# Performance work log

Hardware: AMD Instinct MI355X
Metric: run time of the kernel (lower is better)

Reference implementation:

```python
import jax, jax.numpy as jnp
import numpy as np

SAMPLE_NUMS = 9
VIEW_RANGE = 2      # args.max_turn_view_range
TEMP = 0.07         # args.temperature
AVG_EPS = 1e-6      # BertAVG eps
COS_EPS = 1e-8      # torch.cosine_similarity eps


def setup_inputs() -> dict:
    key = jax.random.key(0)
    k0, k1, k2 = jax.random.split(key, 3)
    G, S, H = 8, 512, 768            # groups, max_seq_length, hidden_size
    B = G * SAMPLE_NUMS              # 72 flattened dialogues
    self_output = jax.random.normal(k0, (B, S, H), dtype=jnp.float32)
    attention_mask = jnp.ones((B, S), dtype=jnp.float32)
    qa_ids = jax.random.randint(k1, (B, S), 0, 4, dtype=jnp.int32)
    turn_ids = jnp.sort(jax.random.randint(k2, (B, S), 0, 16, dtype=jnp.int32), axis=-1)
    labels = jnp.zeros((G, SAMPLE_NUMS), dtype=jnp.float32).at[:, 0].set(1.0)
    return {"self_output": self_output, "attention_mask": attention_mask,
            "labels": labels, "qa_ids": qa_ids, "turn_ids": turn_ids}


def _masked_avg(x, m):
    # BertAVG: sum over seq of x*m / (sum(m) + eps)   x:[B,S,H] m:[B,S]
    return jnp.sum(x * m[..., None], axis=1) / (jnp.sum(m, axis=1, keepdims=True) + AVG_EPS)


def _cos(x, y):
    # torch.cosine_similarity over last dim, eps-clamped norms
    dot = jnp.sum(x * y, axis=-1)
    nx = jnp.maximum(jnp.linalg.norm(x, axis=-1), COS_EPS)
    ny = jnp.maximum(jnp.linalg.norm(y, axis=-1), COS_EPS)
    c = dot / (nx * ny)
    c = jnp.where(c == 1.0, jnp.nan, c)   # cos[cos==1] = nan
    return c / TEMP


def _calc_loss(pred, labels):
    return -jnp.nanmean(jax.nn.log_softmax(pred, axis=-1) * labels)


def reference(self_output, attention_mask, labels, qa_ids, turn_ids):
    H = self_output.shape[-1]
    # role masks from qa_ids
    q_mask = ((qa_ids == 1) | (qa_ids == 2)).astype(self_output.dtype)
    a_mask = ((qa_ids == 0) | (qa_ids == 2)).astype(self_output.dtype)
    n_mask = (qa_ids == 3).astype(self_output.dtype)
    q_am = attention_mask * q_mask
    a_am = attention_mask * a_mask
    n_am = attention_mask * n_mask
    q_so = self_output * q_am[..., None]   # [B,S,H]
    a_so = self_output * a_am[..., None]
    n_so = self_output * n_am[..., None]
    # role-masked cross scores [B,S,S]
    q_w = jnp.einsum('bsh,bth->bst', q_so, a_so + n_so)
    a_w = jnp.einsum('bsh,bth->bst', a_so, q_so + n_so)
    n_w = jnp.einsum('bsh,bth->bst', n_so, q_so + a_so)
    # turn-range band mask: |turn_s - turn_t| <= range
    dt = turn_ids[:, :, None] - turn_ids[:, None, :]
    band = (jnp.abs(dt) <= VIEW_RANGE).astype(self_output.dtype)  # [B,S,S]
    filtered_w = (q_w + a_w + n_w) * band
    # cross outputs
    q_co = jnp.einsum('bst,bth->bsh', filtered_w, q_so)
    a_co = jnp.einsum('bst,bth->bsh', filtered_w, a_so)
    n_co = jnp.einsum('bst,bth->bsh', filtered_w, n_so)
    # masked averages
    q_self = _masked_avg(q_so, q_am)
    q_cross = _masked_avg(q_co, a_am + n_am)
    a_self = _masked_avg(a_so, a_am)
    a_cross = _masked_avg(a_co, q_am + n_am)
    n_self = _masked_avg(n_so, n_am)
    n_cross = _masked_avg(n_co, q_am + a_am)
    # [G, sample_nums, H]
    q_self = q_self.reshape(-1, SAMPLE_NUMS, H)
    q_cross = q_cross.reshape(-1, SAMPLE_NUMS, H)
    a_self = a_self.reshape(-1, SAMPLE_NUMS, H)
    a_cross = a_cross.reshape(-1, SAMPLE_NUMS, H)
    n_self = n_self.reshape(-1, SAMPLE_NUMS, H)
    n_cross = n_cross.reshape(-1, SAMPLE_NUMS, H)
    q_output = q_self[:, 0, :]
    a_output = a_self[:, 0, :]
    n_output = n_self[:, 0, :]
    # vectorized over sample axis (replaces the python loop + stack)
    logit_q = _cos(q_self, q_cross)  # [G, sample_nums]
    logit_a = _cos(a_self, a_cross)
    logit_n = _cos(n_self, n_cross)
    stage_loss = (_calc_loss(logit_a, labels) + _calc_loss(logit_q, labels)
                  + _calc_loss(logit_n, labels)) / 3.0
    return (stage_loss, q_output, a_output, n_output)
```

## Files before the change

### kernel.cpp

```cpp
#include <hip/hip_runtime.h>
#include <math.h>

#define BB 72
#define SS 512
#define HH 768
#define GG 8
#define SN 9
#define VR 2
#define NT 16
#define NPART 16


__device__ float g_G [(size_t)BB * NT * 4 * HH];
__device__ float g_Wm[(size_t)BB * NT * 4 * HH];
__device__ float g_snum[BB * 3 * HH];
__device__ float g_xpart[(size_t)BB * NPART * 3 * HH];
__device__ float g_logits[3 * BB];

__device__ __forceinline__ void class_masks(float am, int id, float& qv, float& av, float& nv) {
    qv = (id == 1 || id == 2) ? am : 0.0f;
    av = (id == 0 || id == 2) ? am : 0.0f;
    nv = (id == 3) ? am : 0.0f;
}

__global__ __launch_bounds__(384) void k_g(const float* __restrict__ x,
                                           const float* __restrict__ am,
                                           const int* __restrict__ qa,
                                           const int* __restrict__ turn) {
    __shared__ int   tn[SS];
    __shared__ float c2s[SS];
    __shared__ int   idvs[SS];
    __shared__ float Gh[4 * HH];

    const int u = blockIdx.x, b = blockIdx.y;
    const int tid = threadIdx.x;
    const int grp = (tid >= 192) ? 1 : 0;
    const int lt  = tid - grp * 192;

    for (int i = tid; i < SS; i += 384) tn[i] = turn[b * SS + i];
    __syncthreads();

    int L = 0, R = SS;
    while (L < R) { int m = (L + R) >> 1; if (tn[m] < u) L = m + 1; else R = m; }
    const int beg = L;
    L = beg; R = SS;
    while (L < R) { int m = (L + R) >> 1; if (tn[m] <= u) L = m + 1; else R = m; }
    const int end = L;

    for (int i = beg + tid; i < end; i += 384) {
        float a = am[b * SS + i]; c2s[i] = a * a;
        idvs[i] = qa[b * SS + i];
    }
    __syncthreads();

    float4 acc[4];
#pragma unroll
    for (int i = 0; i < 4; ++i) acc[i] = make_float4(0.f, 0.f, 0.f, 0.f);

    const float* xb = x + (size_t)b * SS * HH + lt * 4;
    for (int s0 = beg; s0 < end; s0 += 16) {
        float4 v[8];
#pragma unroll
        for (int k = 0; k < 8; ++k) {
            const int ss = s0 + 2 * k + grp;
            v[k] = (ss < end) ? *(const float4*)(xb + (size_t)ss * HH)
                              : make_float4(0.f, 0.f, 0.f, 0.f);
        }
#pragma unroll
        for (int k = 0; k < 8; ++k) {
            const int ss = s0 + 2 * k + grp;
            if (ss < end) {
                const float cc = c2s[ss];
                const int id = idvs[ss];
                const float4 xv = v[k];
                if (id == 0) { acc[0].x += xv.x * cc; acc[0].y += xv.y * cc;
                               acc[0].z += xv.z * cc; acc[0].w += xv.w * cc; }
                else if (id == 1) { acc[1].x += xv.x * cc; acc[1].y += xv.y * cc;
                                    acc[1].z += xv.z * cc; acc[1].w += xv.w * cc; }
                else if (id == 2) { acc[2].x += xv.x * cc; acc[2].y += xv.y * cc;
                                    acc[2].z += xv.z * cc; acc[2].w += xv.w * cc; }
                else { acc[3].x += xv.x * cc; acc[3].y += xv.y * cc;
                       acc[3].z += xv.z * cc; acc[3].w += xv.w * cc; }
            }
        }
    }

    if (grp == 1) {
#pragma unroll
        for (int i = 0; i < 4; ++i)
            *(float4*)&Gh[i * HH + lt * 4] = acc[i];
    }
    __syncthreads();
    if (grp == 0) {
        float* go = g_G + ((size_t)(b * NT + u) * 4) * HH + lt * 4;
#pragma unroll
        for (int i = 0; i < 4; ++i) {
            const float4 o = *(const float4*)&Gh[i * HH + lt * 4];
            float4 s;
            s.x = acc[i].x + o.x; s.y = acc[i].y + o.y;
            s.z = acc[i].z + o.z; s.w = acc[i].w + o.w;
            *(float4*)(go + (size_t)i * HH) = s;
        }
    }
}

__global__ __launch_bounds__(256) void k_w() {
    __shared__ float Gl[NT * 4 * 192];
    const int qh = blockIdx.x, b = blockIdx.y, tid = threadIdx.x;

    for (int idx = tid * 4; idx < NT * 4 * 192; idx += 1024) {
        const int u = idx / 768, rem = idx % 768;
        const int i = rem / 192, hh = rem % 192;
        *(float4*)&Gl[idx] =
            *(const float4*)(g_G + ((size_t)(b * NT + u) * 4 + i) * HH + qh * 192 + hh);
    }
    __syncthreads();

    for (int idx = tid * 4; idx < NT * 4 * 192; idx += 1024) {
        const int v = idx / 768, rem = idx % 768;
        const int i = rem / 192, hh = rem % 192;
        const int ulo = (v - VR < 0) ? 0 : v - VR;
        const int uhi = (v + VR > NT - 1) ? NT - 1 : v + VR;
        float4 s = make_float4(0.f, 0.f, 0.f, 0.f);
        for (int u = ulo; u <= uhi; ++u) {
            const float4 gv = *(const float4*)&Gl[(u * 4 + i) * 192 + hh];
            s.x += gv.x; s.y += gv.y; s.z += gv.z; s.w += gv.w;
        }
        *(float4*)(g_Wm + ((size_t)(b * NT + v) * 4 + i) * HH + qh * 192 + hh) = s;
    }

    if (tid < 48) {
        const int hh = tid * 4;
        float4 t0 = make_float4(0.f,0.f,0.f,0.f), t1 = t0, t2 = t0, t3 = t0;
        for (int u = 0; u < NT; ++u) {
            const float4 g0 = *(const float4*)&Gl[(u * 4 + 0) * 192 + hh];
            const float4 g1 = *(const float4*)&Gl[(u * 4 + 1) * 192 + hh];
            const float4 g2 = *(const float4*)&Gl[(u * 4 + 2) * 192 + hh];
            const float4 g3 = *(const float4*)&Gl[(u * 4 + 3) * 192 + hh];
            t0.x += g0.x; t0.y += g0.y; t0.z += g0.z; t0.w += g0.w;
            t1.x += g1.x; t1.y += g1.y; t1.z += g1.z; t1.w += g1.w;
            t2.x += g2.x; t2.y += g2.y; t2.z += g2.z; t2.w += g2.w;
            t3.x += g3.x; t3.y += g3.y; t3.z += g3.z; t3.w += g3.w;
        }
        float4 oq, oa, on;
        oq.x = t1.x + t2.x; oq.y = t1.y + t2.y; oq.z = t1.z + t2.z; oq.w = t1.w + t2.w;
        oa.x = t0.x + t2.x; oa.y = t0.y + t2.y; oa.z = t0.z + t2.z; oa.w = t0.w + t2.w;
        on = t3;
        *(float4*)(g_snum + (size_t)(b * 3 + 0) * HH + qh * 192 + hh) = oq;
        *(float4*)(g_snum + (size_t)(b * 3 + 1) * HH + qh * 192 + hh) = oa;
        *(float4*)(g_snum + (size_t)(b * 3 + 2) * HH + qh * 192 + hh) = on;
    }
}

__global__ __launch_bounds__(256) void k_ct(const float* __restrict__ x,
                                            const float* __restrict__ am,
                                            const int* __restrict__ qa,
                                            const int* __restrict__ turn) {
    __shared__ float red[4][3 * HH];
    __shared__ int   tnb[32];
    __shared__ float amb[32];
    __shared__ int   idb[32];

    const int b = blockIdx.y, ts = blockIdx.x, T0 = ts * 32;
    const int tid = threadIdx.x, w = tid >> 6, lane = tid & 63;
    if (tid < 32) {
        tnb[tid] = turn[b * SS + T0 + tid];
        amb[tid] = am[b * SS + T0 + tid];
        idb[tid] = qa[b * SS + T0 + tid];
    }
    __syncthreads();

    const float* xb = x + (size_t)b * SS * HH;
    float4 xt[8][3];
#pragma unroll
    for (int it = 0; it < 8; ++it) {
        const float* xr = xb + (size_t)(T0 + w * 8 + it) * HH + lane * 4;
        xt[it][0] = *(const float4*)(xr + 0);
        xt[it][1] = *(const float4*)(xr + 256);
        xt[it][2] = *(const float4*)(xr + 512);
    }

    float4 Wr[4][3];
    int curv = tnb[w * 8];
    {
        const float* Wg = g_Wm + ((size_t)(b * NT + curv) * 4) * HH + lane * 4;
#pragma unroll
        for (int i = 0; i < 4; ++i) {
            Wr[i][0] = *(const float4*)(Wg + (size_t)i * HH + 0);
            Wr[i][1] = *(const float4*)(Wg + (size_t)i * HH + 256);
            Wr[i][2] = *(const float4*)(Wg + (size_t)i * HH + 512);
        }
    }

    float xn[3][12];
#pragma unroll
    for (int c = 0; c < 3; ++c)
#pragma unroll
        for (int k = 0; k < 12; ++k) xn[c][k] = 0.0f;

#pragma unroll
    for (int it = 0; it < 8; ++it) {
        const int tl = w * 8 + it;
        const int v = tnb[tl];
        if (v != curv) {
            curv = v;
            const float* Wg = g_Wm + ((size_t)(b * NT + v) * 4) * HH + lane * 4;
#pragma unroll
            for (int i = 0; i < 4; ++i) {
                Wr[i][0] = *(const float4*)(Wg + (size_t)i * HH + 0);
                Wr[i][1] = *(const float4*)(Wg + (size_t)i * HH + 256);
                Wr[i][2] = *(const float4*)(Wg + (size_t)i * HH + 512);
            }
        }
        float d[4];
#pragma unroll
        for (int i = 0; i < 4; ++i) {
            float s = 0;
#pragma unroll
            for (int ch = 0; ch < 3; ++ch) {
                s += xt[it][ch].x * Wr[i][ch].x + xt[it][ch].y * Wr[i][ch].y
                   + xt[it][ch].z * Wr[i][ch].z + xt[it][ch].w * Wr[i][ch].w;
            }
            d[i] = s;
        }
#pragma unroll
        for (int off = 32; off; off >>= 1) {
#pragma unroll
            for (int i = 0; i < 4; ++i) d[i] += __shfl_xor(d[i], off);
        }
        float qt, at, nt; class_masks(amb[tl], idb[tl], qt, at, nt);
        const float ant = at + nt, qnt = qt + nt, qat = qt + at;
        const float Sqq = d[1] + d[2], Sqa = d[2], Saa = d[0] + d[2], Snn = d[3];
        const float cwq = qt * (ant * Sqa + qnt * Saa + qat * Snn);
        const float cwa = at * (ant * Sqq + qnt * Sqa + qat * Snn);
        const float cwn = nt * (ant * (Sqq + Sqa) + qnt * (Sqa + Saa));
#pragma unroll
        for (int ch = 0; ch < 3; ++ch) {
            const float4 xv = xt[it][ch];
            xn[0][ch * 4 + 0] += cwq * xv.x; xn[0][ch * 4 + 1] += cwq * xv.y;
            xn[0][ch * 4 + 2] += cwq * xv.z; xn[0][ch * 4 + 3] += cwq * xv.w;
            xn[1][ch * 4 + 0] += cwa * xv.x; xn[1][ch * 4 + 1] += cwa * xv.y;
            xn[1][ch * 4 + 2] += cwa * xv.z; xn[1][ch * 4 + 3] += cwa * xv.w;
            xn[2][ch * 4 + 0] += cwn * xv.x; xn[2][ch * 4 + 1] += cwn * xv.y;
            xn[2][ch * 4 + 2] += cwn * xv.z; xn[2][ch * 4 + 3] += cwn * xv.w;
        }
    }

#pragma unroll
    for (int c = 0; c < 3; ++c) {
#pragma unroll
        for (int ch = 0; ch < 3; ++ch) {
            float4 o;
            o.x = xn[c][ch * 4 + 0]; o.y = xn[c][ch * 4 + 1];
            o.z = xn[c][ch * 4 + 2]; o.w = xn[c][ch * 4 + 3];
            *(float4*)&red[w][c * HH + ch * 256 + lane * 4] = o;
        }
    }
    __syncthreads();
    float* xo = g_xpart + (size_t)(b * NPART + ts) * 3 * HH;
    for (int idx = tid * 4; idx < 3 * HH; idx += 1024) {
        float4 r0 = *(float4*)&red[0][idx];
        float4 r1 = *(float4*)&red[1][idx];
        float4 r2 = *(float4*)&red[2][idx];
        float4 r3 = *(float4*)&red[3][idx];
        float4 o;
        o.x = r0.x + r1.x + r2.x + r3.x;
        o.y = r0.y + r1.y + r2.y + r3.y;
        o.z = r0.z + r1.z + r2.z + r3.z;
        o.w = r0.w + r1.w + r2.w + r3.w;
        *(float4*)(xo + idx) = o;
    }
}

__global__ void k_cos(const float* __restrict__ am, const int* __restrict__ qa,
                      float* __restrict__ out) {
    const int c = blockIdx.x, b = blockIdx.y, tid = threadIdx.x;
    const int wave = tid >> 6, lane = tid & 63;
    __shared__ float redd[4][3];
    __shared__ float sD[3];

    float q = 0, a = 0, n = 0;
    for (int s = tid; s < SS; s += 256) {
        float m = am[b * SS + s]; int id = qa[b * SS + s];
        float qv, av, nv; class_masks(m, id, qv, av, nv);
        q += qv; a += av; n += nv;
    }
#pragma unroll
    for (int off = 32; off; off >>= 1) {
        q += __shfl_down(q, off); a += __shfl_down(a, off); n += __shfl_down(n, off);
    }
    if (lane == 0) { redd[wave][0] = q; redd[wave][1] = a; redd[wave][2] = n; }
    __syncthreads();
    if (tid == 0) {
        float Q = 0, A = 0, N = 0;
#pragma unroll
        for (int w = 0; w < 4; ++w) { Q += redd[w][0]; A += redd[w][1]; N += redd[w][2]; }
        sD[0] = Q; sD[1] = A; sD[2] = N;
    }
    __syncthreads();
    const float Dq = sD[0], Da = sD[1], Dn = sD[2];
    const float Dself = (c == 0) ? Dq : ((c == 1) ? Da : Dn);
    const float Dcross = (c == 0) ? (Da + Dn) : ((c == 1) ? (Dq + Dn) : (Dq + Da));
    const float invS = 1.0f / (Dself + 1e-6f), invC = 1.0f / (Dcross + 1e-6f);

    float dot = 0, n1 = 0, n2 = 0;
#pragma unroll
    for (int j = 0; j < 3; ++j) {
        const int h = tid + j * 256;
        float sv = g_snum[(size_t)(b * 3 + c) * HH + h];
        float cv = 0;
        const float* xp = g_xpart + ((size_t)b * NPART * 3 + c) * HH + h;
#pragma unroll
        for (int p = 0; p < NPART; ++p) cv += xp[(size_t)p * 3 * HH];
        sv *= invS; cv *= invC;
        dot += sv * cv; n1 += sv * sv; n2 += cv * cv;
        if (b % SN == 0)
            out[1 + ((size_t)c * GG + b / SN) * HH + h] = sv;
    }
#pragma unroll
    for (int off = 32; off; off >>= 1) {
        dot += __shfl_down(dot, off); n1 += __shfl_down(n1, off); n2 += __shfl_down(n2, off);
    }
    __shared__ float red2[4][3];
    if (lane == 0) { red2[wave][0] = dot; red2[wave][1] = n1; red2[wave][2] = n2; }
    __syncthreads();
    if (tid == 0) {
        float D = 0, N1 = 0, N2 = 0;
#pragma unroll
        for (int w = 0; w < 4; ++w) { D += red2[w][0]; N1 += red2[w][1]; N2 += red2[w][2]; }
        float nx = fmaxf(sqrtf(N1), 1e-8f);
        float ny = fmaxf(sqrtf(N2), 1e-8f);
        float cc = D / (nx * ny);
        if (cc == 1.0f) cc = __uint_as_float(0x7FC00000u);
        g_logits[c * BB + b] = cc / 0.07f;
    }
}

__global__ void k_loss(const float* __restrict__ labels, float* __restrict__ out) {
    __shared__ float rs[24];
    __shared__ int rc[24];
    const int tid = threadIdx.x;
    if (tid < 24) {
        int c = tid / GG, g = tid % GG;
        float lg[SN]; bool anynan = false;
        for (int j = 0; j < SN; ++j) {
            float v = g_logits[c * BB + g * SN + j];
            lg[j] = v;
            anynan = anynan || isnan(v);
        }
        float ssum = 0; int cnt = 0;
        if (!anynan) {
            float m = -1e30f;
            for (int j = 0; j < SN; ++j) m = fmaxf(m, lg[j]);
            float se = 0;
            for (int j = 0; j < SN; ++j) se += expf(lg[j] - m);
            float lse = m + logf(se);
            for (int j = 0; j < SN; ++j) ssum += (lg[j] - lse) * labels[g * SN + j];
            cnt = SN;
        }
        rs[tid] = ssum; rc[tid] = cnt;
    }
    __syncthreads();
    if (tid == 0) {
        float total = 0;
        for (int c = 0; c < 3; ++c) {
            float s = 0; int n = 0;
            for (int g = 0; g < GG; ++g) { s += rs[c * GG + g]; n += rc[c * GG + g]; }
            total += -(s / (float)n);
        }
        out[0] = total / 3.0f;
    }
}

extern "C" void kernel_launch(void* const* d_in, const int* in_sizes, int n_in,
                              void* d_out, int out_size, void* d_ws, size_t ws_size,
                              hipStream_t stream) {
    const float* x      = (const float*)d_in[0];
    const float* am     = (const float*)d_in[1];
    const float* labels = (const float*)d_in[2];
    const int*   qa     = (const int*)d_in[3];
    const int*   turn   = (const int*)d_in[4];
    float* out = (float*)d_out;

    k_g   <<<dim3(NT, BB),      384, 0, stream>>>(x, am, qa, turn);
    k_w   <<<dim3(4, BB),       256, 0, stream>>>();
    k_ct  <<<dim3(SS / 32, BB), 256, 0, stream>>>(x, am, qa, turn);
    k_cos <<<dim3(3, BB),       256, 0, stream>>>(am, qa, out);
    k_loss<<<dim3(1),           64,  0, stream>>>(labels, out);
}
```

Before: 242.9 us.

## Partition k_ct blocks by turn value to load W once per block

k_ct now assigns one block per (turn value, dialogue) and finds that turn's token range in the sorted turn_ids with a binary search over shared memory. Each block loads its W row set once and streams the tokens of its turn with a double-buffered prefetch of x rows, instead of fixed 32-token blocks that reload W whenever the turn changes. The aim is fewer redundant W loads and less register pressure. The cost is load imbalance, since turn lengths vary and some blocks may get little or no work, and a loop whose trip count is not known at compile time.

```diff
diff --git a/kernel.cpp b/kernel.cpp
--- a/kernel.cpp
+++ b/kernel.cpp
@@ -8,7 +8,7 @@
 #define SN 9
 #define VR 2
 #define NT 16
-#define NPART 16
+#define NPART NT
 
 
 __device__ float g_G [(size_t)BB * NT * 4 * HH];
@@ -157,40 +157,25 @@
                                             const int* __restrict__ qa,
                                             const int* __restrict__ turn) {
     __shared__ float red[4][3 * HH];
-    __shared__ int   tnb[32];
-    __shared__ float amb[32];
-    __shared__ int   idb[32];
-
-    const int b = blockIdx.y, ts = blockIdx.x, T0 = ts * 32;
+    __shared__ int   tns[SS];
+    __shared__ float ams[SS];
+    __shared__ int   ids[SS];
+
+    const int v = blockIdx.x, b = blockIdx.y;
     const int tid = threadIdx.x, w = tid >> 6, lane = tid & 63;
-    if (tid < 32) {
-        tnb[tid] = turn[b * SS + T0 + tid];
-        amb[tid] = am[b * SS + T0 + tid];
-        idb[tid] = qa[b * SS + T0 + tid];
-    }
-    __syncthreads();
-
-    const float* xb = x + (size_t)b * SS * HH;
-    float4 xt[8][3];
-#pragma unroll
-    for (int it = 0; it < 8; ++it) {
-        const float* xr = xb + (size_t)(T0 + w * 8 + it) * HH + lane * 4;
-        xt[it][0] = *(const float4*)(xr + 0);
-        xt[it][1] = *(const float4*)(xr + 256);
-        xt[it][2] = *(const float4*)(xr + 512);
-    }
-
-    float4 Wr[4][3];
-    int curv = tnb[w * 8];
-    {
-        const float* Wg = g_Wm + ((size_t)(b * NT + curv) * 4) * HH + lane * 4;
-#pragma unroll
-        for (int i = 0; i < 4; ++i) {
-            Wr[i][0] = *(const float4*)(Wg + (size_t)i * HH + 0);
-            Wr[i][1] = *(const float4*)(Wg + (size_t)i * HH + 256);
-            Wr[i][2] = *(const float4*)(Wg + (size_t)i * HH + 512);
-        }
-    }
+    for (int i = tid; i < SS; i += 256) {
+        tns[i] = turn[b * SS + i];
+        ams[i] = am[b * SS + i];
+        ids[i] = qa[b * SS + i];
+    }
+    __syncthreads();
+
+    int L = 0, R = SS;
+    while (L < R) { int m = (L + R) >> 1; if (tns[m] < v) L = m + 1; else R = m; }
+    const int beg = L;
+    L = beg; R = SS;
+    while (L < R) { int m = (L + R) >> 1; if (tns[m] <= v) L = m + 1; else R = m; }
+    const int end = L;
 
     float xn[3][12];
 #pragma unroll
@@ -198,12 +183,9 @@
 #pragma unroll
         for (int k = 0; k < 12; ++k) xn[c][k] = 0.0f;
 
-#pragma unroll
-    for (int it = 0; it < 8; ++it) {
-        const int tl = w * 8 + it;
-        const int v = tnb[tl];
-        if (v != curv) {
-            curv = v;
+    if (beg < end) {
+        float4 Wr[4][3];
+        {
             const float* Wg = g_Wm + ((size_t)(b * NT + v) * 4) * HH + lane * 4;
 #pragma unroll
             for (int i = 0; i < 4; ++i) {
@@ -212,37 +194,59 @@
                 Wr[i][2] = *(const float4*)(Wg + (size_t)i * HH + 512);
             }
         }
-        float d[4];
-#pragma unroll
-        for (int i = 0; i < 4; ++i) {
-            float s = 0;
+        const float* xb = x + (size_t)b * SS * HH + lane * 4;
+
+        int s = beg + w;
+        float4 xA[3];
+        if (s < end) {
+            const float* xr = xb + (size_t)s * HH;
+            xA[0] = *(const float4*)(xr + 0);
+            xA[1] = *(const float4*)(xr + 256);
+            xA[2] = *(const float4*)(xr + 512);
+        }
+        for (; s < end; s += 4) {
+            float4 xB[3];
+            const int sn = s + 4;
+            if (sn < end) {
+                const float* xr = xb + (size_t)sn * HH;
+                xB[0] = *(const float4*)(xr + 0);
+                xB[1] = *(const float4*)(xr + 256);
+                xB[2] = *(const float4*)(xr + 512);
+            }
+            float d[4];
+#pragma unroll
+            for (int i = 0; i < 4; ++i) {
+                float sacc = 0;
+#pragma unroll
+                for (int ch = 0; ch < 3; ++ch) {
+                    sacc += xA[ch].x * Wr[i][ch].x + xA[ch].y * Wr[i][ch].y
+                          + xA[ch].z * Wr[i][ch].z + xA[ch].w * Wr[i][ch].w;
+                }
+                d[i] = sacc;
+            }
+#pragma unroll
+            for (int off = 32; off; off >>= 1) {
+#pragma unroll
+                for (int i = 0; i < 4; ++i) d[i] += __shfl_xor(d[i], off);
+            }
+            float qt, at, nt; class_masks(ams[s], ids[s], qt, at, nt);
+            const float ant = at + nt, qnt = qt + nt, qat = qt + at;
+            const float Sqq = d[1] + d[2], Sqa = d[2], Saa = d[0] + d[2], Snn = d[3];
+            const float cwq = qt * (ant * Sqa + qnt * Saa + qat * Snn);
+            const float cwa = at * (ant * Sqq + qnt * Sqa + qat * Snn);
+            const float cwn = nt * (ant * (Sqq + Sqa) + qnt * (Sqa + Saa));
 #pragma unroll
             for (int ch = 0; ch < 3; ++ch) {
-                s += xt[it][ch].x * Wr[i][ch].x + xt[it][ch].y * Wr[i][ch].y
-                   + xt[it][ch].z * Wr[i][ch].z + xt[it][ch].w * Wr[i][ch].w;
-            }
-            d[i] = s;
-        }
-#pragma unroll
-        for (int off = 32; off; off >>= 1) {
-#pragma unroll
-            for (int i = 0; i < 4; ++i) d[i] += __shfl_xor(d[i], off);
-        }
-        float qt, at, nt; class_masks(amb[tl], idb[tl], qt, at, nt);
-        const float ant = at + nt, qnt = qt + nt, qat = qt + at;
-        const float Sqq = d[1] + d[2], Sqa = d[2], Saa = d[0] + d[2], Snn = d[3];
-        const float cwq = qt * (ant * Sqa + qnt * Saa + qat * Snn);
-        const float cwa = at * (ant * Sqq + qnt * Sqa + qat * Snn);
-        const float cwn = nt * (ant * (Sqq + Sqa) + qnt * (Sqa + Saa));
-#pragma unroll
-        for (int ch = 0; ch < 3; ++ch) {
-            const float4 xv = xt[it][ch];
-            xn[0][ch * 4 + 0] += cwq * xv.x; xn[0][ch * 4 + 1] += cwq * xv.y;
-            xn[0][ch * 4 + 2] += cwq * xv.z; xn[0][ch * 4 + 3] += cwq * xv.w;
-            xn[1][ch * 4 + 0] += cwa * xv.x; xn[1][ch * 4 + 1] += cwa * xv.y;
-            xn[1][ch * 4 + 2] += cwa * xv.z; xn[1][ch * 4 + 3] += cwa * xv.w;
-            xn[2][ch * 4 + 0] += cwn * xv.x; xn[2][ch * 4 + 1] += cwn * xv.y;
-            xn[2][ch * 4 + 2] += cwn * xv.z; xn[2][ch * 4 + 3] += cwn * xv.w;
+                const float4 xv = xA[ch];
+                xn[0][ch * 4 + 0] += cwq * xv.x; xn[0][ch * 4 + 1] += cwq * xv.y;
+                xn[0][ch * 4 + 2] += cwq * xv.z; xn[0][ch * 4 + 3] += cwq * xv.w;
+                xn[1][ch * 4 + 0] += cwa * xv.x; xn[1][ch * 4 + 1] += cwa * xv.y;
+                xn[1][ch * 4 + 2] += cwa * xv.z; xn[1][ch * 4 + 3] += cwa * xv.w;
+                xn[2][ch * 4 + 0] += cwn * xv.x; xn[2][ch * 4 + 1] += cwn * xv.y;
+                xn[2][ch * 4 + 2] += cwn * xv.z; xn[2][ch * 4 + 3] += cwn * xv.w;
+            }
+#pragma unroll
+            for (int ch = 0; ch < 3; ++ch) xA[ch] = xB[ch];
         }
     }
 
@@ -257,7 +261,7 @@
         }
     }
     __syncthreads();
-    float* xo = g_xpart + (size_t)(b * NPART + ts) * 3 * HH;
+    float* xo = g_xpart + (size_t)(b * NPART + v) * 3 * HH;
     for (int idx = tid * 4; idx < 3 * HH; idx += 1024) {
         float4 r0 = *(float4*)&red[0][idx];
         float4 r1 = *(float4*)&red[1][idx];
@@ -382,9 +386,9 @@
     const int*   turn   = (const int*)d_in[4];
     float* out = (float*)d_out;
 
-    k_g   <<<dim3(NT, BB),      384, 0, stream>>>(x, am, qa, turn);
-    k_w   <<<dim3(4, BB),       256, 0, stream>>>();
-    k_ct  <<<dim3(SS / 32, BB), 256, 0, stream>>>(x, am, qa, turn);
-    k_cos <<<dim3(3, BB),       256, 0, stream>>>(am, qa, out);
-    k_loss<<<dim3(1),           64,  0, stream>>>(labels, out);
-}
+    k_g   <<<dim3(NT, BB), 384, 0, stream>>>(x, am, qa, turn);
+    k_w   <<<dim3(4, BB),  256, 0, stream>>>();
+    k_ct  <<<dim3(NT, BB), 256, 0, stream>>>(x, am, qa, turn);
+    k_cos <<<dim3(3, BB),  256, 0, stream>>>(am, qa, out);
+    k_loss<<<dim3(1),      64,  0, stream>>>(labels, out);
+}
```

Measured after the change: 232.6 us. 4.3% less time.
